# Kernel tuning notes

Measured on AMD Instinct MI355X. Metric: run time of the kernel, lower is better.

Reference implementation:

```python
import jax, jax.numpy as jnp
import numpy as np
import math

B = 1048576
BG_RES = 512
NUM_LEVELS = 2
POWER = 4
MIPNOISE = 0.5
INIT_VAL = -2.0


def cube_face_uv(v):
    # v: [N,3] direction vectors. OpenGL cubemap face convention
    # (faces: 0:+x 1:-x 2:+y 3:-y 4:+z 5:-z), as used by nvdiffrast 'cube'.
    x, y, z = v[:, 0], v[:, 1], v[:, 2]
    ax, ay, az = jnp.abs(x), jnp.abs(y), jnp.abs(z)
    is_x = (ax >= ay) & (ax >= az)
    is_y = (~is_x) & (ay >= az)
    face = jnp.where(is_x, jnp.where(x >= 0, 0, 1),
                     jnp.where(is_y, jnp.where(y >= 0, 2, 3),
                               jnp.where(z >= 0, 4, 5))).astype(jnp.int32)
    ma = jnp.where(is_x, ax, jnp.where(is_y, ay, az))
    sc = jnp.where(is_x, jnp.where(x >= 0, -z, z),
                   jnp.where(is_y, x, jnp.where(z >= 0, x, -x)))
    tc = jnp.where(is_x, -y, jnp.where(is_y, jnp.where(y >= 0, z, -z), -y))
    u = 0.5 * (sc / ma + 1.0)
    t = 0.5 * (tc / ma + 1.0)
    return face, u, t


def build_pyramid(tex):
    # tex: [6,R,R,3] -> list of 2x2 box-filtered mips down to 1x1 (nvdiffrast style)
    levels = [tex]
    t = tex
    while t.shape[1] > 1:
        R = t.shape[1]
        t = t.reshape(6, R // 2, 2, R // 2, 2, 3).mean(axis=(2, 4))
        levels.append(t)
    return levels


def bilinear(tex, face, u, v):
    # tex: [6,R,R,3]; face/u/v: [N]. Clamp-to-edge bilinear per selected face.
    R = tex.shape[1]
    x = u * R - 0.5
    y = v * R - 0.5
    x0f = jnp.floor(x); y0f = jnp.floor(y)
    fx = (x - x0f)[:, None]; fy = (y - y0f)[:, None]
    x0 = jnp.clip(x0f.astype(jnp.int32), 0, R - 1)
    y0 = jnp.clip(y0f.astype(jnp.int32), 0, R - 1)
    x1 = jnp.clip(x0f.astype(jnp.int32) + 1, 0, R - 1)
    y1 = jnp.clip(y0f.astype(jnp.int32) + 1, 0, R - 1)
    flat = tex.reshape(6 * R * R, 3)
    base = face * (R * R)
    g00 = flat[base + y0 * R + x0]
    g01 = flat[base + y0 * R + x1]
    g10 = flat[base + y1 * R + x0]
    g11 = flat[base + y1 * R + x1]
    return ((1 - fx) * (1 - fy) * g00 + fx * (1 - fy) * g01 +
            (1 - fx) * fy * g10 + fx * fy * g11)


def sample_cubemap(tex6, face, u, v, mip):
    # trilinear: bilinear in two adjacent mips, lerp by fractional mip level
    levels = build_pyramid(tex6)
    lmax = float(len(levels) - 1)
    m = jnp.clip(mip, 0.0, lmax)
    out = jnp.zeros((face.shape[0], 3), tex6.dtype)
    for l, t in enumerate(levels):
        wl = jnp.clip(1.0 - jnp.abs(m - l), 0.0, 1.0)  # (1-f)/f trilinear weights
        out = out + wl[:, None] * bilinear(t, face, u, v)
    return out


def setup_inputs() -> dict:
    key = jax.random.key(0)
    k1, k2, k3, k4, k5 = jax.random.split(key, 5)
    viewdirs = jax.random.normal(k1, (B, 3), dtype=jnp.float32)
    viewdirs = viewdirs / jnp.linalg.norm(viewdirs, axis=-1, keepdims=True)
    saSample = jax.random.normal(k2, (B,), dtype=jnp.float32)
    noise_u = jax.random.uniform(k3, (B,), dtype=jnp.float32)
    # parameters (init_val*ones/(num_levels-i) in torch; perturbed for nontrivial grads)
    bg_mat0 = (INIT_VAL * jnp.ones((1, 6, 128, 128, 3), jnp.float32)
               + 0.1 * jax.random.normal(k4, (1, 6, 128, 128, 3), jnp.float32))
    bg_mat1 = (INIT_VAL / 2.0 * jnp.ones((1, 6, 512, 512, 3), jnp.float32)
               + 0.1 * jax.random.normal(k5, (1, 6, 512, 512, 3), jnp.float32))
    return {
        "viewdirs": viewdirs,
        "saSample": saSample,
        "noise_u": noise_u,
        "bg_mat0": bg_mat0,
        "bg_mat1": bg_mat1,
        "brightness": jnp.asarray(0.0, jnp.float32),
        "mul": jnp.asarray(1.0, jnp.float32),
        "mipbias": jnp.asarray(0.5, jnp.float32),
    }


def reference(viewdirs, saSample, noise_u, bg_mat0, bg_mat1, brightness, mul, mipbias):
    h = w = BG_RES  # from bg_mats[-1]
    # sa2mip
    distortion = 1.0 / jnp.max(jnp.abs(viewdirs), axis=-1)  # 1/||u||_inf
    saTexel = distortion / h / w
    miplevel = ((saSample - jnp.log(saTexel)) / math.log(POWER) / 2.0
                + mipbias + MIPNOISE * noise_u)
    miplevel = jnp.maximum(miplevel, 0.0)

    face, u, t = cube_face_uv(viewdirs)
    sumemb = sample_cubemap(bg_mat0[0], face, u, t, miplevel)  # mip 1 (128)
    sumemb = sumemb + sample_cubemap(bg_mat1[0], face, u, t, miplevel)  # mip 0 (512)

    # activation == 'identity' branch: exp(x).clip(0.01, 1000)
    img = jnp.clip(jnp.exp(jnp.clip(brightness, -1.0, 2.0) + mul * sumemb), 0.01, 1000.0)
    return img
```

## Files before the change

### kernel.cpp

```cpp
#include <hip/hip_runtime.h>
#include <math.h>


#define NPYR1_4 524286
#define FPB 557052
#define NFP 36780

__device__ __constant__ int OFFS0[7] = {0, 24576, 30720, 32256, 32640, 32736, 32760};
__device__ __constant__ int OFFS1[9] = {0, 393216, 491520, 516096, 522240,
                                        523776, 524160, 524256, 524280};
static const int H_OFFS0[7] = {0, 24576, 30720, 32256, 32640, 32736, 32760};
static const int H_OFFS1[9] = {0, 393216, 491520, 516096, 522240,
                               523776, 524160, 524256, 524280};

__device__ __constant__ int FPO1C[7] = {0, 25350, 31884, 33618, 34104, 34254, 34308};
__device__ __constant__ int FPO0C[5] = {34332, 36066, 36552, 36702, 36756};

__device__ __constant__ int C_SEG_START[13] = {0, 25350, 31884, 33618, 34104, 34254,
                                               34308, 34332, 36066, 36552, 36702,
                                               36756, 36780};
__device__ __constant__ int C_SEG_R[12] = {64, 32, 16, 8, 4, 2, 1, 16, 8, 4, 2, 1};
__device__ __constant__ int C_SEG_SRC[12] = {491520, 516096, 522240, 523776, 524160,
                                             524256, 524280, 555006, 556542, 556926,
                                             557022, 557046};

struct PyrArgs {
    const void* src;
    float4* dst[5];
    int R;
    int tpf;
    int T;
    int nlev;
    int rgba;
};

__global__ __launch_bounds__(256) void pyr_kernel(PyrArgs a0, PyrArgs a1, int split) {
    __shared__ float4 A[32 * 32];
    __shared__ float4 Bb[16 * 16];

    PyrArgs a = (blockIdx.x < (unsigned)split) ? a0 : a1;
    int bid = (blockIdx.x < (unsigned)split) ? blockIdx.x : blockIdx.x - split;

    const int tpf = a.tpf;
    const int face = bid / (tpf * tpf);
    const int tif = bid - face * tpf * tpf;
    const int ty = tif / tpf, tx = tif - (tif / tpf) * tpf;
    const int T = a.T, R = a.R;
    const int tid = threadIdx.x;
    const int baseY = ty * T, baseX = tx * T;

    const int total = T * T;
    if (a.rgba) {
        const float4* src = (const float4*)a.src;
        for (int idx = tid; idx < total; idx += 256) {
            int r = idx / T, c = idx - (idx / T) * T;
            A[r * T + c] = src[(size_t)(face * R + baseY + r) * R + baseX + c];
        }
    } else {
        const float* src = (const float*)a.src;
        for (int idx = tid; idx < total; idx += 256) {
            int r = idx / T, c = idx - (idx / T) * T;
            const float* p = src + ((size_t)(face * R + baseY + r) * R + baseX + c) * 3;
            A[r * T + c] = make_float4(p[0], p[1], p[2], 0.f);
        }
    }
    __syncthreads();

    float4* cur = A;
    float4* nxt = Bb;
    int curT = T;
    for (int l = 0; l < a.nlev; ++l) {
        const int nT = curT >> 1;
        const int Rg = R >> (l + 1);
        const int tb = T >> (l + 1);
        float4* dst = a.dst[l];
        const int n = nT * nT;
        for (int idx = tid; idx < n; idx += 256) {
            int ly = idx / nT, lx = idx - (idx / nT) * nT;
            float4 q00 = cur[(2 * ly) * curT + 2 * lx];
            float4 q01 = cur[(2 * ly) * curT + 2 * lx + 1];
            float4 q10 = cur[(2 * ly + 1) * curT + 2 * lx];
            float4 q11 = cur[(2 * ly + 1) * curT + 2 * lx + 1];
            float4 s = make_float4(0.25f * (q00.x + q01.x + q10.x + q11.x),
                                   0.25f * (q00.y + q01.y + q10.y + q11.y),
                                   0.25f * (q00.z + q01.z + q10.z + q11.z), 0.f);
            nxt[ly * nT + lx] = s;
            dst[(size_t)(face * Rg + ty * tb + ly) * Rg + tx * tb + lx] = s;
        }
        __syncthreads();
        float4* tmp = cur; cur = nxt; nxt = tmp;
        curT = nT;
    }
}

__global__ __launch_bounds__(256) void fpify_kernel(const float4* __restrict__ ws4,
                                                    float4* __restrict__ fp4) {
    int t = blockIdx.x * 256 + threadIdx.x;
    if (t >= NFP) return;
    int s = 0;
#pragma unroll
    for (int k = 1; k <= 12; ++k)
        if (t >= C_SEG_START[k]) s = k;
    int local = t - C_SEG_START[s];
    int R = C_SEG_R[s];
    int per1 = R + 1;
    int per = per1 * per1;
    int face = local / per;
    int rem = local - face * per;
    int j = rem / per1;
    int i = rem - j * per1;
    const float4* fb = ws4 + C_SEG_SRC[s] + (size_t)face * R * R;
    int x0 = max(i - 1, 0), x1 = min(i, R - 1);
    int y0 = max(j - 1, 0), y1 = min(j, R - 1);
    float4 q00 = fb[y0 * R + x0];
    float4 q01 = fb[y0 * R + x1];
    float4 q10 = fb[y1 * R + x0];
    float4 q11 = fb[y1 * R + x1];
    size_t d = (size_t)t * 4;
    fp4[d]     = make_float4(q00.x, q00.y, q00.z, q01.x);
    fp4[d + 1] = make_float4(q01.y, q01.z, q10.x, q10.y);
    fp4[d + 2] = make_float4(q10.z, q11.x, q11.y, q11.z);
}

__device__ __forceinline__ void sample_level_fp(const float4* __restrict__ fp, int R,
                                                int face, float u, float v, float o[3]) {
    float xf = u * (float)R - 0.5f;
    float yf = v * (float)R - 0.5f;
    float x0f = floorf(xf), y0f = floorf(yf);
    float fx = xf - x0f, fy = yf - y0f;
    int i = min(max((int)x0f + 1, 0), R);
    int j = min(max((int)y0f + 1, 0), R);
    int per1 = R + 1;
    size_t base = (size_t)((face * per1 + j) * per1 + i) * 4;
    float4 A  = fp[base];
    float4 Bq = fp[base + 1];
    float4 C  = fp[base + 2];
    float w00 = (1.f - fx) * (1.f - fy);
    float w01 = fx * (1.f - fy);
    float w10 = (1.f - fx) * fy;
    float w11 = fx * fy;
    o[0] = w00 * A.x + w01 * A.w + w10 * Bq.z + w11 * C.y;
    o[1] = w00 * A.y + w01 * Bq.x + w10 * Bq.w + w11 * C.z;
    o[2] = w00 * A.z + w01 * Bq.y + w10 * C.x + w11 * C.w;
}

__device__ __forceinline__ void bilin4(const float4* __restrict__ tex, int R,
                                       int face, float u, float v, float o[3]) {
    float xf = u * (float)R - 0.5f;
    float yf = v * (float)R - 0.5f;
    float x0f = floorf(xf), y0f = floorf(yf);
    float fx = xf - x0f, fy = yf - y0f;
    int xi = (int)x0f, yi = (int)y0f;
    int x0 = min(max(xi, 0), R - 1);
    int x1 = min(max(xi + 1, 0), R - 1);
    int y0 = min(max(yi, 0), R - 1);
    int y1 = min(max(yi + 1, 0), R - 1);
    const float4* base = tex + (size_t)face * R * R;
    float4 p00 = base[y0 * R + x0];
    float4 p01 = base[y0 * R + x1];
    float4 p10 = base[y1 * R + x0];
    float4 p11 = base[y1 * R + x1];
    float w00 = (1.f - fx) * (1.f - fy);
    float w01 = fx * (1.f - fy);
    float w10 = (1.f - fx) * fy;
    float w11 = fx * fy;
    o[0] = w00 * p00.x + w01 * p01.x + w10 * p10.x + w11 * p11.x;
    o[1] = w00 * p00.y + w01 * p01.y + w10 * p10.y + w11 * p11.y;
    o[2] = w00 * p00.z + w01 * p01.z + w10 * p10.z + w11 * p11.z;
}

__device__ __forceinline__ void bilin3(const float* __restrict__ tex, int R,
                                       int face, float u, float v, float o[3]) {
    float xf = u * (float)R - 0.5f;
    float yf = v * (float)R - 0.5f;
    float x0f = floorf(xf), y0f = floorf(yf);
    float fx = xf - x0f, fy = yf - y0f;
    int xi = (int)x0f, yi = (int)y0f;
    int x0 = min(max(xi, 0), R - 1);
    int x1 = min(max(xi + 1, 0), R - 1);
    int y0 = min(max(yi, 0), R - 1);
    int y1 = min(max(yi + 1, 0), R - 1);
    const float* base = tex + (size_t)face * R * R * 3;
    const float* p00 = base + (y0 * R + x0) * 3;
    const float* p01 = base + (y0 * R + x1) * 3;
    const float* p10 = base + (y1 * R + x0) * 3;
    const float* p11 = base + (y1 * R + x1) * 3;
    float w00 = (1.f - fx) * (1.f - fy);
    float w01 = fx * (1.f - fy);
    float w10 = (1.f - fx) * fy;
    float w11 = fx * fy;
#pragma unroll
    for (int c = 0; c < 3; ++c)
        o[c] = w00 * p00[c] + w01 * p01[c] + w10 * p10[c] + w11 * p11[c];
}

__device__ __forceinline__ void sample_pyr(const float* __restrict__ base_tex,
                                           const float4* __restrict__ pyr,
                                           const int* offs,
                                           const float4* __restrict__ fp4,
                                           const int* fpoffs,
                                           int lmax, int R0,
                                           int face, float u, float v, float mip,
                                           float o[3]) {
    float m = fminf(fmaxf(mip, 0.f), (float)lmax);
    float l0f = floorf(m);
    int l0 = (int)l0f;
    float f = m - l0f;
    float c0[3];
    if (l0 >= 3)
        sample_level_fp(fp4 + (size_t)fpoffs[l0 - 3] * 4, R0 >> l0, face, u, v, c0);
    else if (l0 == 0)
        bilin3(base_tex, R0, face, u, v, c0);
    else
        bilin4(pyr + offs[l0 - 1], R0 >> l0, face, u, v, c0);
    if (f > 0.f && l0 < lmax) {
        float c1[3];
        int l1 = l0 + 1;
        if (l1 >= 3)
            sample_level_fp(fp4 + (size_t)fpoffs[l1 - 3] * 4, R0 >> l1, face, u, v, c1);
        else
            bilin4(pyr + offs[l1 - 1], R0 >> l1, face, u, v, c1);
        float w0 = 1.f - f;
#pragma unroll
        for (int c = 0; c < 3; ++c) o[c] = w0 * c0[c] + f * c1[c];
    } else {
#pragma unroll
        for (int c = 0; c < 3; ++c) o[c] = c0[c];
    }
}

__global__ __launch_bounds__(256) void sample_kernel(
    const float* __restrict__ vd, const float* __restrict__ sa,
    const float* __restrict__ nu, const float* __restrict__ tex0,
    const float* __restrict__ tex1, const float* __restrict__ sb,
    const float* __restrict__ sm, const float* __restrict__ smb,
    const float4* __restrict__ pyr0, const float4* __restrict__ pyr1,
    const float4* __restrict__ fp4, float* __restrict__ out, int n) {
    int i = blockIdx.x * 256 + threadIdx.x;
    if (i >= n) return;

    float x = vd[3 * i + 0];
    float y = vd[3 * i + 1];
    float z = vd[3 * i + 2];
    float ax = fabsf(x), ay = fabsf(y), az = fabsf(z);

    bool is_x = (ax >= ay) && (ax >= az);
    bool is_y = (!is_x) && (ay >= az);

    int face;
    float ma, sc, tc;
    if (is_x) {
        face = (x >= 0.f) ? 0 : 1;
        ma = ax;
        sc = (x >= 0.f) ? -z : z;
        tc = -y;
    } else if (is_y) {
        face = (y >= 0.f) ? 2 : 3;
        ma = ay;
        sc = x;
        tc = (y >= 0.f) ? z : -z;
    } else {
        face = (z >= 0.f) ? 4 : 5;
        ma = az;
        sc = (z >= 0.f) ? x : -x;
        tc = -y;
    }
    float u = 0.5f * (sc / ma + 1.f);
    float t = 0.5f * (tc / ma + 1.f);

    float distortion = 1.f / ma;
    float saTexel = distortion / 512.f / 512.f;
    float mip = (sa[i] - logf(saTexel)) / 1.3862943611198906f / 2.0f +
                smb[0] + 0.5f * nu[i];
    mip = fmaxf(mip, 0.f);

    float s0[3], s1[3];
    sample_pyr(tex0, pyr0, OFFS0, fp4, FPO0C, 7, 128, face, u, t, mip, s0);
    sample_pyr(tex1, pyr1, OFFS1, fp4, FPO1C, 9, 512, face, u, t, mip, s1);

    float b = fminf(fmaxf(sb[0], -1.f), 2.f);
    float mul = sm[0];
#pragma unroll
    for (int c = 0; c < 3; ++c) {
        float e = expf(b + mul * (s0[c] + s1[c]));
        out[3 * i + c] = fminf(fmaxf(e, 0.01f), 1000.f);
    }
}

extern "C" void kernel_launch(void* const* d_in, const int* in_sizes, int n_in,
                              void* d_out, int out_size, void* d_ws, size_t ws_size,
                              hipStream_t stream) {
    const float* vd = (const float*)d_in[0];
    const float* sa = (const float*)d_in[1];
    const float* nu = (const float*)d_in[2];
    const float* tex0 = (const float*)d_in[3];
    const float* tex1 = (const float*)d_in[4];
    const float* br = (const float*)d_in[5];
    const float* mu = (const float*)d_in[6];
    const float* mb = (const float*)d_in[7];
    float* out = (float*)d_out;

    float4* pyr1 = (float4*)d_ws;
    float4* pyr0 = pyr1 + NPYR1_4;
    float4* fp4 = pyr1 + FPB;

    const int B = in_sizes[1];

    PyrArgs a0{}, a1{};
    a0.src = tex1; a0.R = 512; a0.tpf = 16; a0.T = 32; a0.nlev = 5; a0.rgba = 0;
    for (int l = 0; l < 5; ++l) a0.dst[l] = pyr1 + H_OFFS1[l];
    a1.src = tex0; a1.R = 128; a1.tpf = 4; a1.T = 32; a1.nlev = 5; a1.rgba = 0;
    for (int l = 0; l < 5; ++l) a1.dst[l] = pyr0 + H_OFFS0[l];
    int split1 = 6 * 16 * 16;
    int grid1 = split1 + 6 * 4 * 4;
    hipLaunchKernelGGL(pyr_kernel, dim3(grid1), dim3(256), 0, stream, a0, a1, split1);

    PyrArgs b0{}, b1{};
    b0.src = pyr1 + H_OFFS1[4]; b0.R = 16; b0.tpf = 1; b0.T = 16; b0.nlev = 4; b0.rgba = 1;
    for (int l = 0; l < 4; ++l) b0.dst[l] = pyr1 + H_OFFS1[5 + l];
    b1.src = pyr0 + H_OFFS0[4]; b1.R = 4; b1.tpf = 1; b1.T = 4; b1.nlev = 2; b1.rgba = 1;
    for (int l = 0; l < 2; ++l) b1.dst[l] = pyr0 + H_OFFS0[5 + l];
    hipLaunchKernelGGL(pyr_kernel, dim3(12), dim3(256), 0, stream, b0, b1, 6);

    hipLaunchKernelGGL(fpify_kernel, dim3((NFP + 255) / 256), dim3(256), 0, stream,
                       (const float4*)d_ws, fp4);

    int grid = (B + 255) / 256;
    hipLaunchKernelGGL(sample_kernel, dim3(grid), dim3(256), 0, stream,
                       vd, sa, nu, tex0, tex1, br, mu, mb, pyr0, pyr1, fp4, out, B);
}
```

Measured before the change: 141.3 us.

## Fuse pyramid tail into fp-packing kernel and add warp-uniform fast sampling path

Merges the second pyramid launch and the fp-packing kernel into one tail kernel, where 12 blocks build the small mip levels in shared memory and pack them directly. The remaining blocks pack the larger levels standalone, so one launch is removed. The first pyramid pass now loads raw RGB with float4 vector loads and does the first downsample inline. The sampler gains a fast path, used when the whole wavefront's mip level lies in 3..6, that samples only the four needed packed levels. Fast-math reciprocal, log and exp replace the precise versions, which adds small precision risk and wavefront divergence checks.

```diff
diff --git a/kernel.cpp b/kernel.cpp
--- a/kernel.cpp
+++ b/kernel.cpp
@@ -5,74 +5,77 @@
 #define NPYR1_4 524286
 #define FPB 557052
 #define NFP 36780
+#define NSTANDALONE 35988
 
 __device__ __constant__ int OFFS0[7] = {0, 24576, 30720, 32256, 32640, 32736, 32760};
 __device__ __constant__ int OFFS1[9] = {0, 393216, 491520, 516096, 522240,
                                         523776, 524160, 524256, 524280};
-static const int H_OFFS0[7] = {0, 24576, 30720, 32256, 32640, 32736, 32760};
-static const int H_OFFS1[9] = {0, 393216, 491520, 516096, 522240,
-                               523776, 524160, 524256, 524280};
+static const int H_OFFS0[5] = {0, 24576, 30720, 32256, 32640};
+static const int H_OFFS1[5] = {0, 393216, 491520, 516096, 522240};
 
 __device__ __constant__ int FPO1C[7] = {0, 25350, 31884, 33618, 34104, 34254, 34308};
 __device__ __constant__ int FPO0C[5] = {34332, 36066, 36552, 36702, 36756};
 
-__device__ __constant__ int C_SEG_START[13] = {0, 25350, 31884, 33618, 34104, 34254,
-                                               34308, 34332, 36066, 36552, 36702,
-                                               36756, 36780};
-__device__ __constant__ int C_SEG_R[12] = {64, 32, 16, 8, 4, 2, 1, 16, 8, 4, 2, 1};
-__device__ __constant__ int C_SEG_SRC[12] = {491520, 516096, 522240, 523776, 524160,
-                                             524256, 524280, 555006, 556542, 556926,
-                                             557022, 557046};
+__device__ __constant__ int FPB1T[4] = {33618, 34104, 34254, 34308};
+__device__ __constant__ int FPB0T[2] = {36702, 36756};
+
+__device__ __constant__ int S_START[7] = {0, 25350, 31884, 33618, 35352, 35838, 35988};
+__device__ __constant__ int S_R[6]     = {64, 32, 16, 16, 8, 4};
+__device__ __constant__ int S_SRC[6]   = {491520, 516096, 522240, 555006, 556542, 556926};
+__device__ __constant__ int S_DST[6]   = {0, 25350, 31884, 34332, 36066, 36552};
 
 struct PyrArgs {
-    const void* src;
+    const float* src;
     float4* dst[5];
     int R;
     int tpf;
-    int T;
-    int nlev;
-    int rgba;
 };
 
 __global__ __launch_bounds__(256) void pyr_kernel(PyrArgs a0, PyrArgs a1, int split) {
-    __shared__ float4 A[32 * 32];
-    __shared__ float4 Bb[16 * 16];
+    __shared__ float raw[32 * 96];
+    __shared__ float4 A[16 * 16];
+    __shared__ float4 Bb[8 * 8];
 
     PyrArgs a = (blockIdx.x < (unsigned)split) ? a0 : a1;
     int bid = (blockIdx.x < (unsigned)split) ? blockIdx.x : blockIdx.x - split;
 
-    const int tpf = a.tpf;
+    const int tpf = a.tpf, R = a.R;
     const int face = bid / (tpf * tpf);
     const int tif = bid - face * tpf * tpf;
     const int ty = tif / tpf, tx = tif - (tif / tpf) * tpf;
-    const int T = a.T, R = a.R;
     const int tid = threadIdx.x;
-    const int baseY = ty * T, baseX = tx * T;
-
-    const int total = T * T;
-    if (a.rgba) {
-        const float4* src = (const float4*)a.src;
-        for (int idx = tid; idx < total; idx += 256) {
-            int r = idx / T, c = idx - (idx / T) * T;
-            A[r * T + c] = src[(size_t)(face * R + baseY + r) * R + baseX + c];
-        }
-    } else {
-        const float* src = (const float*)a.src;
-        for (int idx = tid; idx < total; idx += 256) {
-            int r = idx / T, c = idx - (idx / T) * T;
-            const float* p = src + ((size_t)(face * R + baseY + r) * R + baseX + c) * 3;
-            A[r * T + c] = make_float4(p[0], p[1], p[2], 0.f);
-        }
+    const int baseY = ty * 32, baseX = tx * 32;
+
+    const float4* src4 = (const float4*)a.src;
+    float4* raw4 = (float4*)raw;
+    for (int idx = tid; idx < 768; idx += 256) {
+        int r = idx / 24, c = idx - (idx / 24) * 24;
+        size_t fidx = ((size_t)(face * R + baseY + r) * R + baseX) * 3;
+        raw4[r * 24 + c] = src4[fidx / 4 + c];
+    }
+    __syncthreads();
+
+    {
+        int Rg = R >> 1;
+        float4* dst = a.dst[0];
+        int ly = tid >> 4, lx = tid & 15;
+        const float* r0 = raw + (2 * ly) * 96 + 6 * lx;
+        const float* r1 = r0 + 96;
+        float4 s = make_float4(0.25f * (r0[0] + r0[3] + r1[0] + r1[3]),
+                               0.25f * (r0[1] + r0[4] + r1[1] + r1[4]),
+                               0.25f * (r0[2] + r0[5] + r1[2] + r1[5]), 0.f);
+        A[tid] = s;
+        dst[(size_t)(face * Rg + ty * 16 + ly) * Rg + tx * 16 + lx] = s;
     }
     __syncthreads();
 
     float4* cur = A;
     float4* nxt = Bb;
-    int curT = T;
-    for (int l = 0; l < a.nlev; ++l) {
+    int curT = 16;
+    for (int l = 1; l < 5; ++l) {
         const int nT = curT >> 1;
         const int Rg = R >> (l + 1);
-        const int tb = T >> (l + 1);
+        const int tb = 32 >> (l + 1);
         float4* dst = a.dst[l];
         const int n = nT * nT;
         for (int idx = tid; idx < n; idx += 256) {
@@ -93,33 +96,86 @@
     }
 }
 
-__global__ __launch_bounds__(256) void fpify_kernel(const float4* __restrict__ ws4,
-                                                    float4* __restrict__ fp4) {
-    int t = blockIdx.x * 256 + threadIdx.x;
-    if (t >= NFP) return;
-    int s = 0;
-#pragma unroll
-    for (int k = 1; k <= 12; ++k)
-        if (t >= C_SEG_START[k]) s = k;
-    int local = t - C_SEG_START[s];
-    int R = C_SEG_R[s];
-    int per1 = R + 1;
-    int per = per1 * per1;
-    int face = local / per;
-    int rem = local - face * per;
-    int j = rem / per1;
-    int i = rem - j * per1;
-    const float4* fb = ws4 + C_SEG_SRC[s] + (size_t)face * R * R;
-    int x0 = max(i - 1, 0), x1 = min(i, R - 1);
-    int y0 = max(j - 1, 0), y1 = min(j, R - 1);
-    float4 q00 = fb[y0 * R + x0];
-    float4 q01 = fb[y0 * R + x1];
-    float4 q10 = fb[y1 * R + x0];
-    float4 q11 = fb[y1 * R + x1];
-    size_t d = (size_t)t * 4;
-    fp4[d]     = make_float4(q00.x, q00.y, q00.z, q01.x);
-    fp4[d + 1] = make_float4(q01.y, q01.z, q10.x, q10.y);
-    fp4[d + 2] = make_float4(q10.z, q11.x, q11.y, q11.z);
+__global__ __launch_bounds__(256) void tail_fp_kernel(const float4* __restrict__ ws4,
+                                                      float4* __restrict__ fp4) {
+    __shared__ float4 A[16 * 16];
+    __shared__ float4 Bb[8 * 8];
+    const int tid = threadIdx.x;
+    const int b = blockIdx.x;
+
+    if (b < 12) {
+        const int isP0 = (b >= 6) ? 1 : 0;
+        const int face = isP0 ? (b - 6) : b;
+        const int R0 = isP0 ? 4 : 16;
+        const int nlev = isP0 ? 2 : 4;
+        const int srcoff = isP0 ? (NPYR1_4 + 32640) : 522240;
+        const float4* src = ws4 + srcoff + (size_t)face * R0 * R0;
+        for (int idx = tid; idx < R0 * R0; idx += 256) A[idx] = src[idx];
+        __syncthreads();
+
+        float4* cur = A;
+        float4* nxt = Bb;
+        int curT = R0;
+        for (int l = 0; l < nlev; ++l) {
+            const int nT = curT >> 1;
+            for (int idx = tid; idx < nT * nT; idx += 256) {
+                int ly = idx / nT, lx = idx - (idx / nT) * nT;
+                float4 q00 = cur[(2 * ly) * curT + 2 * lx];
+                float4 q01 = cur[(2 * ly) * curT + 2 * lx + 1];
+                float4 q10 = cur[(2 * ly + 1) * curT + 2 * lx];
+                float4 q11 = cur[(2 * ly + 1) * curT + 2 * lx + 1];
+                nxt[ly * nT + lx] =
+                    make_float4(0.25f * (q00.x + q01.x + q10.x + q11.x),
+                                0.25f * (q00.y + q01.y + q10.y + q11.y),
+                                0.25f * (q00.z + q01.z + q10.z + q11.z), 0.f);
+            }
+            __syncthreads();
+            const int Rl = nT, per1 = Rl + 1;
+            const int fpbase = (isP0 ? FPB0T[l] : FPB1T[l]) + face * per1 * per1;
+            for (int idx = tid; idx < per1 * per1; idx += 256) {
+                int j = idx / per1, i = idx - (idx / per1) * per1;
+                int x0 = max(i - 1, 0), x1 = min(i, Rl - 1);
+                int y0 = max(j - 1, 0), y1 = min(j, Rl - 1);
+                float4 q00 = nxt[y0 * Rl + x0];
+                float4 q01 = nxt[y0 * Rl + x1];
+                float4 q10 = nxt[y1 * Rl + x0];
+                float4 q11 = nxt[y1 * Rl + x1];
+                size_t d = (size_t)(fpbase + idx) * 4;
+                fp4[d]     = make_float4(q00.x, q00.y, q00.z, q01.x);
+                fp4[d + 1] = make_float4(q01.y, q01.z, q10.x, q10.y);
+                fp4[d + 2] = make_float4(q10.z, q11.x, q11.y, q11.z);
+            }
+            __syncthreads();
+            float4* tmp = cur; cur = nxt; nxt = tmp;
+            curT = nT;
+        }
+    } else {
+        int t = (b - 12) * 256 + tid;
+        if (t >= NSTANDALONE) return;
+        int s = 0;
+#pragma unroll
+        for (int k = 1; k <= 5; ++k)
+            if (t >= S_START[k]) s = k;
+        int local = t - S_START[s];
+        int R = S_R[s];
+        int per1 = R + 1;
+        int per = per1 * per1;
+        int face = local / per;
+        int rem = local - face * per;
+        int j = rem / per1;
+        int i = rem - j * per1;
+        const float4* fb = ws4 + S_SRC[s] + (size_t)face * R * R;
+        int x0 = max(i - 1, 0), x1 = min(i, R - 1);
+        int y0 = max(j - 1, 0), y1 = min(j, R - 1);
+        float4 q00 = fb[y0 * R + x0];
+        float4 q01 = fb[y0 * R + x1];
+        float4 q10 = fb[y1 * R + x0];
+        float4 q11 = fb[y1 * R + x1];
+        size_t d = (size_t)(S_DST[s] + local) * 4;
+        fp4[d]     = make_float4(q00.x, q00.y, q00.z, q01.x);
+        fp4[d + 1] = make_float4(q01.y, q01.z, q10.x, q10.y);
+        fp4[d + 2] = make_float4(q10.z, q11.x, q11.y, q11.z);
+    }
 }
 
 __device__ __forceinline__ void sample_level_fp(const float4* __restrict__ fp, int R,
@@ -265,24 +321,47 @@
         sc = (z >= 0.f) ? x : -x;
         tc = -y;
     }
-    float u = 0.5f * (sc / ma + 1.f);
-    float t = 0.5f * (tc / ma + 1.f);
-
-    float distortion = 1.f / ma;
-    float saTexel = distortion / 512.f / 512.f;
-    float mip = (sa[i] - logf(saTexel)) / 1.3862943611198906f / 2.0f +
+    float rma = __frcp_rn(ma);
+    float u = 0.5f * (sc * rma + 1.f);
+    float t = 0.5f * (tc * rma + 1.f);
+
+    float mip = (sa[i] + 12.476649250079015f + __logf(ma)) * 0.36067376022224085f +
                 smb[0] + 0.5f * nu[i];
     mip = fmaxf(mip, 0.f);
 
+    float l0f = floorf(mip);
+    int l0 = (int)l0f;
+    float f = mip - l0f;
+
     float s0[3], s1[3];
-    sample_pyr(tex0, pyr0, OFFS0, fp4, FPO0C, 7, 128, face, u, t, mip, s0);
-    sample_pyr(tex1, pyr1, OFFS1, fp4, FPO1C, 9, 512, face, u, t, mip, s1);
+    bool fast = (l0 >= 3) && (l0 < 7);
+    if (__all(fast)) {
+        int oA = (l0 == 3) ? 0     : (l0 == 4) ? 25350 : (l0 == 5) ? 31884 : 33618;
+        int oB = (l0 == 3) ? 25350 : (l0 == 4) ? 31884 : (l0 == 5) ? 33618 : 34104;
+        int oC = (l0 == 3) ? 34332 : (l0 == 4) ? 36066 : (l0 == 5) ? 36552 : 36702;
+        int oD = (l0 == 3) ? 36066 : (l0 == 4) ? 36552 : (l0 == 5) ? 36702 : 36756;
+        float a0v[3], a1v[3], b0v[3], b1v[3];
+        sample_level_fp(fp4 + (size_t)oA * 4, 512 >> l0, face, u, t, a0v);
+        sample_level_fp(fp4 + (size_t)oB * 4, 512 >> (l0 + 1), face, u, t, a1v);
+        sample_level_fp(fp4 + (size_t)oC * 4, 128 >> l0, face, u, t, b0v);
+        sample_level_fp(fp4 + (size_t)oD * 4, 128 >> (l0 + 1), face, u, t, b1v);
+        float w0 = 1.f - f;
+#pragma unroll
+        for (int c = 0; c < 3; ++c) {
+            s0[c] = w0 * a1v[c] * 0.f + (w0 * a0v[c] + f * a1v[c]);
+            s0[c] = w0 * a0v[c] + f * a1v[c];
+            s1[c] = w0 * b0v[c] + f * b1v[c];
+        }
+    } else {
+        sample_pyr(tex0, pyr0, OFFS0, fp4, FPO0C, 7, 128, face, u, t, mip, s0);
+        sample_pyr(tex1, pyr1, OFFS1, fp4, FPO1C, 9, 512, face, u, t, mip, s1);
+    }
 
     float b = fminf(fmaxf(sb[0], -1.f), 2.f);
     float mul = sm[0];
 #pragma unroll
     for (int c = 0; c < 3; ++c) {
-        float e = expf(b + mul * (s0[c] + s1[c]));
+        float e = __expf(b + mul * (s0[c] + s1[c]));
         out[3 * i + c] = fminf(fmaxf(e, 0.01f), 1000.f);
     }
 }
@@ -307,22 +386,16 @@
     const int B = in_sizes[1];
 
     PyrArgs a0{}, a1{};
-    a0.src = tex1; a0.R = 512; a0.tpf = 16; a0.T = 32; a0.nlev = 5; a0.rgba = 0;
+    a0.src = tex1; a0.R = 512; a0.tpf = 16;
     for (int l = 0; l < 5; ++l) a0.dst[l] = pyr1 + H_OFFS1[l];
-    a1.src = tex0; a1.R = 128; a1.tpf = 4; a1.T = 32; a1.nlev = 5; a1.rgba = 0;
+    a1.src = tex0; a1.R = 128; a1.tpf = 4;
     for (int l = 0; l < 5; ++l) a1.dst[l] = pyr0 + H_OFFS0[l];
     int split1 = 6 * 16 * 16;
     int grid1 = split1 + 6 * 4 * 4;
     hipLaunchKernelGGL(pyr_kernel, dim3(grid1), dim3(256), 0, stream, a0, a1, split1);
 
-    PyrArgs b0{}, b1{};
-    b0.src = pyr1 + H_OFFS1[4]; b0.R = 16; b0.tpf = 1; b0.T = 16; b0.nlev = 4; b0.rgba = 1;
-    for (int l = 0; l < 4; ++l) b0.dst[l] = pyr1 + H_OFFS1[5 + l];
-    b1.src = pyr0 + H_OFFS0[4]; b1.R = 4; b1.tpf = 1; b1.T = 4; b1.nlev = 2; b1.rgba = 1;
-    for (int l = 0; l < 2; ++l) b1.dst[l] = pyr0 + H_OFFS0[5 + l];
-    hipLaunchKernelGGL(pyr_kernel, dim3(12), dim3(256), 0, stream, b0, b1, 6);
-
-    hipLaunchKernelGGL(fpify_kernel, dim3((NFP + 255) / 256), dim3(256), 0, stream,
+    int grid2 = 12 + (NSTANDALONE + 255) / 256;
+    hipLaunchKernelGGL(tail_fp_kernel, dim3(grid2), dim3(256), 0, stream,
                        (const float4*)d_ws, fp4);
 
     int grid = (B + 255) / 256;
```

Result: faster. 119.4 us (-15.5%).
